# Kernel optimization log

Hardware: AMD Instinct MI355X
Metric: run time of the kernel (lower is better)

Reference implementation:

```python
import jax, jax.numpy as jnp
import numpy as np

TAU = 1.0
TOP_K = 2

def setup_inputs() -> dict:
    key = jax.random.key(0)
    ks = jax.random.split(key, 5)
    B, C, H, W, E, GH = 16, 64, 128, 128, 8, 16
    return {
        "x": jax.random.normal(ks[0], (B, C, H, W), dtype=jnp.float32),
        "wg1": jax.random.normal(ks[1], (C, GH), dtype=jnp.float32) * 0.1,
        "bg1": jnp.zeros((GH,), dtype=jnp.float32),
        "wg2": jax.random.normal(ks[2], (GH, E), dtype=jnp.float32) * 0.1,
        "bg2": jnp.zeros((E,), dtype=jnp.float32),
        "w_exp": jax.random.normal(ks[3], (E, C, C, 3, 3), dtype=jnp.float32) * 0.05,
        "b_exp": jnp.zeros((E, C), dtype=jnp.float32),
    }

def reference(x, wg1, bg1, wg2, bg2, w_exp, b_exp):
    B, C, H, W = x.shape
    E = w_exp.shape[0]
    # in_proj / out_proj are Identity (c1 == mid_channels == c2)
    x_proj = x
    # gate: GAP -> Linear -> ReLU -> Linear
    pooled = x_proj.mean(axis=(2, 3))                      # [B, C]
    h = jax.nn.relu(pooled @ wg1 + bg1)                    # [B, GH]
    gate_logits = h @ wg2 + bg2                            # [B, E]
    # soft top-k routing (hard=False)
    gate_probs = jax.nn.softmax(gate_logits / TAU, axis=-1)
    _, topk_idx = jax.lax.top_k(gate_probs, TOP_K)         # [B, K]
    mask = jnp.zeros_like(gate_probs).at[jnp.arange(B)[:, None], topk_idx].set(1.0)
    sparse_probs = gate_probs * mask
    sparse_probs = sparse_probs / (sparse_probs.sum(axis=-1, keepdims=True) + 1e-8)
    # dense all-expert 3x3 conv: fold experts into one grouped-output conv
    kern = w_exp.reshape(E * C, C, 3, 3)                   # [E*C, C, 3, 3]
    y = jax.lax.conv_general_dilated(
        x_proj, kern, window_strides=(1, 1), padding="SAME",
        dimension_numbers=("NCHW", "OIHW", "NCHW"))
    y = y.reshape(B, E, C, H, W) + b_exp[None, :, :, None, None]
    # vectorized weighted combine (replaces the per-sample python loop)
    out = jnp.einsum("be,bechw->bchw", sparse_probs, y)
    # shortcut (c1 == c2)
    return out + x
```

## Files before the change

kernel.cpp:

```cpp
#include <hip/hip_runtime.h>
#include <hip/hip_bf16.h>
#include <math.h>

#define B_  16
#define C_  64
#define HW_ 128
#define E_  8
#define GH_ 16

typedef __attribute__((ext_vector_type(8))) short short8;
typedef __attribute__((ext_vector_type(4))) float float4v;

#define STRIPS 32
#define ROWS_LDS 6
#define COLS_LDS 132
#define XS_SHORTS (ROWS_LDS * COLS_LDS * 32)
#define WB_PER_B (9 * 2 * 4 * 64 * 8)

__global__ __launch_bounds__(256) void pool_kernel(const float* __restrict__ x,
                                                   float* __restrict__ pooled) {
  const int bc = blockIdx.x;
  const float4v* p4 = (const float4v*)(x + (size_t)bc * (HW_ * HW_));
  float4v s4 = {0.f, 0.f, 0.f, 0.f};
  for (int i = threadIdx.x; i < (HW_ * HW_) / 4; i += 256) s4 += p4[i];
  float s = (s4.x + s4.y) + (s4.z + s4.w);
#pragma unroll
  for (int off = 32; off > 0; off >>= 1) s += __shfl_down(s, off, 64);
  __shared__ float red[4];
  if ((threadIdx.x & 63) == 0) red[threadIdx.x >> 6] = s;
  __syncthreads();
  if (threadIdx.x == 0)
    pooled[bc] = (red[0] + red[1] + red[2] + red[3]) * (1.0f / (HW_ * HW_));
}

__global__ __launch_bounds__(256) void combine_kernel(
    const float* __restrict__ w_exp, const float* __restrict__ pooled,
    const float* __restrict__ wg1, const float* __restrict__ bg1,
    const float* __restrict__ wg2, const float* __restrict__ bg2,
    const float* __restrict__ b_exp, __hip_bfloat16* __restrict__ wB,
    float* __restrict__ bcomb) {
  __shared__ float wtmp[8 * 576];
  __shared__ float hsh[GH_];
  __shared__ float psh[E_];
  const int t = threadIdx.x;
  const int b = blockIdx.x >> 3;
  const int cog = blockIdx.x & 7;

  if (t < GH_) {
    float s = bg1[t];
    for (int c = 0; c < C_; c++)
      s = fmaf(pooled[b * C_ + c], wg1[c * GH_ + t], s);
    hsh[t] = fmaxf(s, 0.f);
  }
  __syncthreads();
  if (t == 0) {
    float p[E_];
    float mx = -1e30f;
#pragma unroll
    for (int e = 0; e < E_; e++) {
      float s = bg2[e];
#pragma unroll
      for (int g = 0; g < GH_; g++) s = fmaf(hsh[g], wg2[g * E_ + e], s);
      p[e] = s;
      mx = fmaxf(mx, s);
    }
    float sum = 0.f;
#pragma unroll
    for (int e = 0; e < E_; e++) { p[e] = expf(p[e] - mx); sum += p[e]; }
    const float inv = 1.0f / sum;
#pragma unroll
    for (int e = 0; e < E_; e++) p[e] *= inv;
    int i1 = 0;
#pragma unroll
    for (int e = 1; e < E_; e++) if (p[e] > p[i1]) i1 = e;
    int i2 = -1;
#pragma unroll
    for (int e = 0; e < E_; e++) {
      if (e == i1) continue;
      if (i2 < 0 || p[e] > p[i2]) i2 = e;
    }
    const float denom = p[i1] + p[i2] + 1e-8f;
#pragma unroll
    for (int e = 0; e < E_; e++)
      psh[e] = (e == i1 || e == i2) ? (p[e] / denom) : 0.f;
  }
  __syncthreads();
  float pb[E_];
#pragma unroll
  for (int e = 0; e < E_; e++) pb[e] = psh[e];

  const size_t src0 = (size_t)cog * 8 * 576;
  for (int i = t; i < 4608; i += 256) {
    float s = 0.f;
#pragma unroll
    for (int e = 0; e < E_; e++)
      s = fmaf(pb[e], w_exp[(size_t)e * (C_ * 576) + src0 + i], s);
    wtmp[i] = s;
  }
  __syncthreads();
  for (int i = t; i < 4608; i += 256) {
    const int j = i & 7;
    const int co_l = (i >> 3) & 7;
    const int rest = i >> 6;
    const int quad = rest & 3;
    const int khalf = (rest >> 2) & 1;
    const int pos = rest >> 3;
    const int ci = khalf * 32 + quad * 8 + j;
    const int co = cog * 8 + co_l;
    float v = wtmp[co_l * 576 + ci * 9 + pos];
    if (pos == 4 && co == ci) v += 1.0f;
    wB[(size_t)b * WB_PER_B +
       ((((pos * 2 + khalf) * 4 + quad) * 64) + co) * 8 + j] =
        __float2bfloat16(v);
  }
  if (t < 8) {
    const int co = cog * 8 + t;
    float s = 0.f;
#pragma unroll
    for (int e = 0; e < E_; e++) s = fmaf(pb[e], b_exp[e * C_ + co], s);
    bcomb[b * C_ + co] = s;
  }
}

__global__ __launch_bounds__(512, 4) void conv_kernel(
    const float* __restrict__ x, const __hip_bfloat16* __restrict__ wB,
    const float* __restrict__ bcomb, float* __restrict__ out) {
  __shared__ __align__(16) short xs[XS_SHORTS];

  const int t = threadIdx.x;
  const int blk = blockIdx.x;
  const int xcd = blk & 7;
  const int idx = blk >> 3;
  const int b = xcd * 2 + (idx >> 5);
  const int strip = idx & 31;
  const int ty = strip * 4;

  const int wave = t >> 6;
  const int L = t & 63;
  const int n16 = L & 15;
  const int quad = L >> 4;

  const int s_cq = t & 31;
  const int s_p = t >> 5;

  float bias[4];
#pragma unroll
  for (int nt = 0; nt < 4; nt++) bias[nt] = bcomb[b * C_ + nt * 16 + n16];

  float4v acc[4][4];
#pragma unroll
  for (int mt = 0; mt < 4; mt++)
#pragma unroll
    for (int nt = 0; nt < 4; nt++) acc[mt][nt] = (float4v)0.f;

  for (int h = 0; h < 2; h++) {
    __syncthreads();
#pragma unroll
    for (int r = 0; r < ROWS_LDS; r++) {
      const int gh = ty + r - 1;
      const int ci = h * 32 + s_p * 2;
      float4v vA = {0.f, 0.f, 0.f, 0.f};
      float4v vB = {0.f, 0.f, 0.f, 0.f};
      if ((unsigned)gh < (unsigned)HW_) {
        const float* pA =
            x + (((size_t)(b * C_ + ci) * HW_ + gh) * HW_ + s_cq * 4);
        vA = *(const float4v*)pA;
        vB = *(const float4v*)(pA + HW_ * HW_);
      }
#pragma unroll
      for (int kk = 0; kk < 4; kk++) {
        const int cl = s_cq * 4 + kk + 1;
        const int slot = (s_p >> 2) ^ ((cl >> 1) & 3);
        __hip_bfloat16 ba = __float2bfloat16(vA[kk]);
        __hip_bfloat16 bb = __float2bfloat16(vB[kk]);
        const unsigned pk = (unsigned)*(unsigned short*)&ba |
                            ((unsigned)*(unsigned short*)&bb << 16);
        *(unsigned*)&xs[((r * COLS_LDS + cl) * 4 + slot) * 8 + (s_p & 3) * 2] =
            pk;
      }
      if (t < 32) {
        const int p2 = t & 15;
        const int cl = (t >> 4) ? 129 : 0;
        const int slot = (p2 >> 2) ^ ((cl >> 1) & 3);
        *(unsigned*)&xs[((r * COLS_LDS + cl) * 4 + slot) * 8 + (p2 & 3) * 2] =
            0u;
      }
    }
    __syncthreads();

    const __hip_bfloat16* wBh =
        wB + (size_t)b * WB_PER_B + (size_t)(h * 4 + quad) * 512 + n16 * 8;
    short8 bf[2][4];
#pragma unroll
    for (int nt = 0; nt < 4; nt++)
      bf[0][nt] = *(const short8*)(wBh + nt * 128);

#pragma unroll
    for (int pos = 0; pos < 9; pos++) {
      const int cur = pos & 1;
      if (pos < 8) {
#pragma unroll
        for (int nt = 0; nt < 4; nt++)
          bf[cur ^ 1][nt] =
              *(const short8*)(wBh + (size_t)(pos + 1) * 4096 + nt * 128);
      }
      const int kh = pos / 3;
      const int kw = pos - kh * 3;
      short8 a[4];
#pragma unroll
      for (int mt = 0; mt < 4; mt++) {
        const int mtg = wave * 4 + mt;
        const int lr = (mtg >> 3) + kh;
        const int cl = (mtg & 7) * 16 + n16 + kw;
        const int slot = quad ^ ((cl >> 1) & 3);
        a[mt] = *(const short8*)&xs[((lr * COLS_LDS + cl) * 4 + slot) * 8];
      }
#pragma unroll
      for (int mt = 0; mt < 4; mt++)
#pragma unroll
        for (int nt = 0; nt < 4; nt++)
          acc[mt][nt] = __builtin_amdgcn_mfma_f32_16x16x32_bf16(
              a[mt], bf[cur][nt], acc[mt][nt], 0, 0, 0);
    }
  }

#pragma unroll
  for (int mt = 0; mt < 4; mt++) {
    const int mtg = wave * 4 + mt;
    const int row = ty + (mtg >> 3);
    const int cb = (mtg & 7) * 16 + quad * 4;
#pragma unroll
    for (int nt = 0; nt < 4; nt++) {
      float4v o = acc[mt][nt];
      o.x += bias[nt];
      o.y += bias[nt];
      o.z += bias[nt];
      o.w += bias[nt];
      *(float4v*)(out +
                  ((size_t)(b * C_ + nt * 16 + n16) * HW_ + row) * HW_ + cb) = o;
    }
  }
}

extern "C" void kernel_launch(void* const* d_in, const int* in_sizes, int n_in,
                              void* d_out, int out_size, void* d_ws,
                              size_t ws_size, hipStream_t stream) {
  const float* x     = (const float*)d_in[0];
  const float* wg1   = (const float*)d_in[1];
  const float* bg1   = (const float*)d_in[2];
  const float* wg2   = (const float*)d_in[3];
  const float* bg2   = (const float*)d_in[4];
  const float* w_exp = (const float*)d_in[5];
  const float* b_exp = (const float*)d_in[6];
  float* out = (float*)d_out;

  float* ws = (float*)d_ws;
  float* pooled = ws;
  float* bcomb  = ws + 1024;
  __hip_bfloat16* wB = (__hip_bfloat16*)(ws + 2048);

  pool_kernel<<<B_ * C_, 256, 0, stream>>>(x, pooled);
  combine_kernel<<<B_ * 8, 256, 0, stream>>>(w_exp, pooled, wg1, bg1, wg2, bg2,
                                             b_exp, wB, bcomb);
  conv_kernel<<<512, 512, 0, stream>>>(x, wB, bcomb, out);
}
```

Baseline: 192.8 us.

## Halve conv strip height and pack 8 channels per LDS store

The conv kernel now processes 2 output rows per block with 256 threads and 1024 blocks, instead of 4 rows with 512 threads and 512 blocks. Each thread loads 8 channels of input and writes one packed 16-byte short8 to LDS, replacing the earlier 4-byte stores, with a new swizzle to match. The output store loop is reordered. Smaller strips give more blocks and less LDS per block, but raise the halo overhead (4 rows loaded for 2 output rows, versus 6 for 4) and the number of weight reloads per output.

Result: faster. 188.2 us (-2.4%).

```diff
diff --git a/kernel.cpp b/kernel.cpp
--- a/kernel.cpp
+++ b/kernel.cpp
@@ -11,8 +11,7 @@
 typedef __attribute__((ext_vector_type(8))) short short8;
 typedef __attribute__((ext_vector_type(4))) float float4v;
 
-#define STRIPS 32
-#define ROWS_LDS 6
+#define ROWS_LDS 4
 #define COLS_LDS 132
 #define XS_SHORTS (ROWS_LDS * COLS_LDS * 32)
 #define WB_PER_B (9 * 2 * 4 * 64 * 8)
@@ -122,7 +121,7 @@
   }
 }
 
-__global__ __launch_bounds__(512, 4) void conv_kernel(
+__global__ __launch_bounds__(256, 4) void conv_kernel(
     const float* __restrict__ x, const __hip_bfloat16* __restrict__ wB,
     const float* __restrict__ bcomb, float* __restrict__ out) {
   __shared__ __align__(16) short xs[XS_SHORTS];
@@ -131,18 +130,15 @@
   const int blk = blockIdx.x;
   const int xcd = blk & 7;
   const int idx = blk >> 3;
-  const int b = xcd * 2 + (idx >> 5);
-  const int strip = idx & 31;
-  const int ty = strip * 4;
+  const int b = xcd * 2 + (idx >> 6);
+  const int strip = idx & 63;
+  const int ty = strip * 2;
 
   const int wave = t >> 6;
   const int L = t & 63;
   const int n16 = L & 15;
   const int quad = L >> 4;
 
-  const int s_cq = t & 31;
-  const int s_p = t >> 5;
-
   float bias[4];
 #pragma unroll
   for (int nt = 0; nt < 4; nt++) bias[nt] = bcomb[b * C_ + nt * 16 + n16];
@@ -156,35 +152,43 @@
   for (int h = 0; h < 2; h++) {
     __syncthreads();
 #pragma unroll
-    for (int r = 0; r < ROWS_LDS; r++) {
+    for (int it = 0; it < 2; it++) {
+      const int i = it * 256 + t;
+      const int scq = i & 31;
+      const int grp = (i >> 5) & 3;
+      const int r = i >> 7;
       const int gh = ty + r - 1;
-      const int ci = h * 32 + s_p * 2;
-      float4v vA = {0.f, 0.f, 0.f, 0.f};
-      float4v vB = {0.f, 0.f, 0.f, 0.f};
+      const int ci = h * 32 + grp * 8;
+      float4v v[8];
       if ((unsigned)gh < (unsigned)HW_) {
-        const float* pA =
-            x + (((size_t)(b * C_ + ci) * HW_ + gh) * HW_ + s_cq * 4);
-        vA = *(const float4v*)pA;
-        vB = *(const float4v*)(pA + HW_ * HW_);
-      }
+        const float* p =
+            x + ((size_t)(b * C_ + ci) * HW_ + gh) * HW_ + scq * 4;
+#pragma unroll
+        for (int k = 0; k < 8; k++)
+          v[k] = *(const float4v*)(p + (size_t)k * (HW_ * HW_));
+      } else {
+#pragma unroll
+        for (int k = 0; k < 8; k++) v[k] = (float4v)0.f;
+      }
+      const int slot = grp ^ (scq & 3);
 #pragma unroll
       for (int kk = 0; kk < 4; kk++) {
-        const int cl = s_cq * 4 + kk + 1;
-        const int slot = (s_p >> 2) ^ ((cl >> 1) & 3);
-        __hip_bfloat16 ba = __float2bfloat16(vA[kk]);
-        __hip_bfloat16 bb = __float2bfloat16(vB[kk]);
-        const unsigned pk = (unsigned)*(unsigned short*)&ba |
-                            ((unsigned)*(unsigned short*)&bb << 16);
-        *(unsigned*)&xs[((r * COLS_LDS + cl) * 4 + slot) * 8 + (s_p & 3) * 2] =
-            pk;
-      }
-      if (t < 32) {
-        const int p2 = t & 15;
-        const int cl = (t >> 4) ? 129 : 0;
-        const int slot = (p2 >> 2) ^ ((cl >> 1) & 3);
-        *(unsigned*)&xs[((r * COLS_LDS + cl) * 4 + slot) * 8 + (p2 & 3) * 2] =
-            0u;
-      }
+        const int cl = scq * 4 + kk + 1;
+        short8 pk;
+#pragma unroll
+        for (int k = 0; k < 8; k++) {
+          __hip_bfloat16 bb = __float2bfloat16(v[k][kk]);
+          pk[k] = *(short*)&bb;
+        }
+        *(short8*)&xs[((r * COLS_LDS + cl) * 4 + slot) * 8] = pk;
+      }
+    }
+    if (t < 32) {
+      const int r = t >> 3;
+      const int edge = (t >> 2) & 1;
+      const int slot = t & 3;
+      const int cl = edge ? 129 : 0;
+      *(short8*)&xs[((r * COLS_LDS + cl) * 4 + slot) * 8] = (short8)0;
     }
     __syncthreads();
 
@@ -212,7 +216,7 @@
         const int mtg = wave * 4 + mt;
         const int lr = (mtg >> 3) + kh;
         const int cl = (mtg & 7) * 16 + n16 + kw;
-        const int slot = quad ^ ((cl >> 1) & 3);
+        const int slot = quad ^ (((cl - 1) >> 2) & 3);
         a[mt] = *(const short8*)&xs[((lr * COLS_LDS + cl) * 4 + slot) * 8];
       }
 #pragma unroll
@@ -225,19 +229,24 @@
   }
 
 #pragma unroll
-  for (int mt = 0; mt < 4; mt++) {
-    const int mtg = wave * 4 + mt;
-    const int row = ty + (mtg >> 3);
-    const int cb = (mtg & 7) * 16 + quad * 4;
+  for (int mtp = 0; mtp < 4; mtp += 2) {
 #pragma unroll
     for (int nt = 0; nt < 4; nt++) {
-      float4v o = acc[mt][nt];
-      o.x += bias[nt];
-      o.y += bias[nt];
-      o.z += bias[nt];
-      o.w += bias[nt];
-      *(float4v*)(out +
-                  ((size_t)(b * C_ + nt * 16 + n16) * HW_ + row) * HW_ + cb) = o;
+#pragma unroll
+      for (int d = 0; d < 2; d++) {
+        const int mt = mtp + d;
+        const int mtg = wave * 4 + mt;
+        const int row = ty + (mtg >> 3);
+        const int cb = (mtg & 7) * 16 + quad * 4;
+        float4v o = acc[mt][nt];
+        o.x += bias[nt];
+        o.y += bias[nt];
+        o.z += bias[nt];
+        o.w += bias[nt];
+        *(float4v*)(out +
+                    ((size_t)(b * C_ + nt * 16 + n16) * HW_ + row) * HW_ + cb) =
+            o;
+      }
     }
   }
 }
@@ -262,5 +271,5 @@
   pool_kernel<<<B_ * C_, 256, 0, stream>>>(x, pooled);
   combine_kernel<<<B_ * 8, 256, 0, stream>>>(w_exp, pooled, wg1, bg1, wg2, bg2,
                                              b_exp, wB, bcomb);
-  conv_kernel<<<512, 512, 0, stream>>>(x, wB, bcomb, out);
-}
+  conv_kernel<<<1024, 256, 0, stream>>>(x, wB, bcomb, out);
+}
```
